# Kernel tuning notes

Hardware: AMD Instinct MI355X
Metric: run time of the kernel (lower is better)

The kernel has to match this reference:

```python
import jax, jax.numpy as jnp
import numpy as np


def _pairwise_iou(boxes):
    # boxes: [B, N, 4] in (x1, y1, x2, y2); returns IoU [B, N, N]
    area = (boxes[..., 2] - boxes[..., 0]) * (boxes[..., 3] - boxes[..., 1])  # [B, N]
    lt = jnp.maximum(boxes[:, :, None, :2], boxes[:, None, :, :2])  # [B, N, N, 2]
    rb = jnp.minimum(boxes[:, :, None, 2:], boxes[:, None, :, 2:])
    wh = jnp.clip(rb - lt, 0.0)
    inter = wh[..., 0] * wh[..., 1]  # [B, N, N]
    union = area[:, :, None] + area[:, None, :] - inter
    return inter / jnp.maximum(union, 1e-6)


def setup_inputs() -> dict:
    key = jax.random.key(0)
    kxy, kwh, ks = jax.random.split(key, 3)
    B, N, C = 4, 2048, 4
    xy = jax.random.uniform(kxy, (B, N, 2), dtype=jnp.float32) * 1000.0
    wh = jax.random.uniform(kwh, (B, N, 2), dtype=jnp.float32) * 100.0 + 1.0
    boxes = jnp.concatenate([xy, xy + wh], axis=-1)  # valid xyxy boxes
    scores = jax.random.uniform(ks, (B, C, N), dtype=jnp.float32)
    return {
        "boxes": boxes,
        "scores": scores,
        "iou_threshold": jnp.array([0.5], dtype=jnp.float32),
        "score_threshold": jnp.array([0.05], dtype=jnp.float32),
    }


def reference(boxes, scores, iou_threshold, score_threshold):
    # Greedy NMS-match (mmcv.ops.nms_match semantics), per batch and class.
    # Returns match: [B, C, N] int32 where match[b,c,n] is the index of the
    # group-leader (kept) box that box n belongs to, or -1 if unmatched
    # (i.e. score <= score_threshold).
    B, N, _ = boxes.shape
    C = scores.shape[1]
    thr = iou_threshold[0]
    sthr = score_threshold[0]

    iou = _pairwise_iou(boxes)  # [B, N, N] (shared across classes)
    order = jnp.argsort(-scores, axis=-1)  # [B, C, N], score-descending

    suppressed0 = scores <= sthr            # boxes below score threshold never match
    match0 = jnp.full((B, C, N), -1, jnp.int32)
    b_idx = jnp.arange(B)[:, None]          # [B, 1] for per-batch IoU row gather

    def step(carry, cand):
        # cand: [B, C] box index with next-highest score in each (batch, class)
        suppressed, match = carry           # [B, C, N] bool / int32
        cand_sup = jnp.take_along_axis(suppressed, cand[..., None], axis=-1)[..., 0]
        active = ~cand_sup                  # [B, C]: candidate not yet grouped
        cand_iou = iou[b_idx, cand]         # [B, C, N] IoU of candidate vs all boxes
        matched = active[..., None] & (~suppressed) & (cand_iou > thr)
        match = jnp.where(matched, cand[..., None].astype(jnp.int32), match)
        return (suppressed | matched, match), None

    xs = jnp.moveaxis(order, -1, 0)         # [N, B, C]: sequential greedy order
    (_, match), _ = jax.lax.scan(step, (suppressed0, match0), xs)
    return match
```

## Files before the change

### kernel.cpp

```cpp
#include <hip/hip_runtime.h>
#include <stdint.h>

#define N_   2048
#define NW   64
#define CLS  4
#define B_   4
#define ORD_STRIDE (N_ + 64)

__global__ __launch_bounds__(256) void build_mask(
    const float4* __restrict__ boxes, const float* __restrict__ thr_p,
    uint32_t* __restrict__ ov)
{
  __shared__ float4 sb[N_];
  const int b    = blockIdx.x >> 6;
  const int tile = blockIdx.x & 63;
  const float thr = thr_p[0];
  for (int i = threadIdx.x; i < N_; i += 256) sb[i] = boxes[b * N_ + i];
  __syncthreads();
  const int wv = threadIdx.x >> 6;
  const int ln = threadIdx.x & 63;
  const int r0 = tile * 32 + wv * 8;
  float4 bi[8]; float areai[8];
  #pragma unroll
  for (int rr = 0; rr < 8; ++rr) {
    bi[rr] = sb[r0 + rr];
    areai[rr] = (bi[rr].z - bi[rr].x) * (bi[rr].w - bi[rr].y);
  }
  uint32_t myw[8] = {0, 0, 0, 0, 0, 0, 0, 0};
  for (int g = 0; g < 32; ++g) {
    const float4 bj = sb[g * 64 + ln];
    const float areaj = (bj.z - bj.x) * (bj.w - bj.y);
    const bool sel = ((ln >> 1) == g);
    const bool hi  = (ln & 1);
    #pragma unroll
    for (int rr = 0; rr < 8; ++rr) {
      const float xx1 = fmaxf(bi[rr].x, bj.x);
      const float yy1 = fmaxf(bi[rr].y, bj.y);
      const float xx2 = fminf(bi[rr].z, bj.z);
      const float yy2 = fminf(bi[rr].w, bj.w);
      const float iw = fmaxf(xx2 - xx1, 0.0f);
      const float ih = fmaxf(yy2 - yy1, 0.0f);
      const float inter = iw * ih;
      const float uni = fmaxf(areai[rr] + areaj - inter, 1e-6f);
      const unsigned long long bal = __ballot(inter / uni > thr);
      const uint32_t w = hi ? (uint32_t)(bal >> 32) : (uint32_t)bal;
      if (sel) myw[rr] = w;
    }
  }
  #pragma unroll
  for (int rr = 0; rr < 8; ++rr)
    ov[((size_t)(b * N_ + r0 + rr)) * NW + ln] = myw[rr];
}

__global__ __launch_bounds__(256) void sort_init(
    const float* __restrict__ scores, const float* __restrict__ sthr_p,
    int* __restrict__ order, int* __restrict__ rk, uint32_t* __restrict__ sup0ws)
{
  __shared__ unsigned long long sp[N_];
  __shared__ uint32_t sup_l[NW];
  __shared__ int cnt_s;
  const int bc = blockIdx.x;
  const float sthr = sthr_p[0];
  const float* s = scores + (size_t)bc * N_;
  for (int i = threadIdx.x; i < N_; i += 256) {
    const float v = s[i];
    uint32_t u = __float_as_uint(v);
    u = (u >> 31) ? ~u : (u | 0x80000000u);
    sp[i] = ((unsigned long long)u << 32) | (uint32_t)(~(uint32_t)i);
    const unsigned long long bal = __ballot(v <= sthr);
    if ((threadIdx.x & 63) == 0) {
      sup_l[(i >> 5)]     = (uint32_t)bal;
      sup_l[(i >> 5) + 1] = (uint32_t)(bal >> 32);
    }
  }
  for (int size = 2; size <= N_; size <<= 1) {
    for (int stride = size >> 1; stride > 0; stride >>= 1) {
      __syncthreads();
      for (int t = threadIdx.x; t < N_ / 2; t += 256) {
        const int pos = 2 * t - (t & (stride - 1));
        const bool desc = ((t & (size >> 1)) == 0);
        const unsigned long long a = sp[pos], c = sp[pos + stride];
        if (desc != (a > c)) { sp[pos] = c; sp[pos + stride] = a; }
      }
    }
  }
  __syncthreads();
  if (threadIdx.x == 0) {
    int c2 = 0;
    for (int w = 0; w < NW; ++w) c2 += __popc(sup_l[w]);
    cnt_s = N_ - c2;
  }
  __syncthreads();
  const int cnt = cnt_s;
  const int last = (cnt > 0) ? (int)~(uint32_t)sp[cnt - 1] : 0;
  int* ord_o = order + (size_t)bc * ORD_STRIDE;
  int* rk_o  = rk    + (size_t)bc * N_;
  for (int i = threadIdx.x; i < N_; i += 256) {
    const int idx = (int)~(uint32_t)sp[i];
    ord_o[i] = (i < cnt || cnt == 0) ? idx : last;
    rk_o[idx] = i;
  }
  for (int i = N_ + threadIdx.x; i < ORD_STRIDE; i += 256) ord_o[i] = last;
  if (threadIdx.x < NW) sup0ws[bc * NW + threadIdx.x] = sup_l[threadIdx.x];
}


#define C_(r,b,s) \
  "v_and_b32 v36, v" #r ", v34\n\t"              \
  "v_lshlrev_b32 v38, 8, v" #s "\n\t"            \
  "v_cmp_ne_u32 s[46:47], 0, v36\n\t"            \
  "v_add_u32 v38, v38, v33\n\t"                  \
  "v_bfe_u32 v44, v" #s ", 5, 6\n\t"             \
  "s_and_b64 s[46:47], s[46:47], s[46:47]\n\t"   \
  "s_cselect_b32 s40, 0, -1\n\t"                 \
  "global_load_dword v" #r ", v38, %[B]\n\t"     \
  "v_and_b32 v37, s40, v" #b "\n\t"              \
  "v_or_b32 v34, v34, v37\n\t"                   \
  "v_cmp_eq_u32 s[48:49], v44, v32\n\t"          \
  "v_cndmask_b32 v37, 0, v45, s[48:49]\n\t"      \
  "v_lshlrev_b32 v" #b ", v" #s ", v37\n\t"

#define P_(r,b,s) \
  "v_lshlrev_b32 v38, 8, v" #s "\n\t"            \
  "v_add_u32 v38, v38, v33\n\t"                  \
  "global_load_dword v" #r ", v38, %[B]\n\t"     \
  "v_bfe_u32 v44, v" #s ", 5, 6\n\t"             \
  "v_cmp_eq_u32 s[48:49], v44, v32\n\t"          \
  "v_cndmask_b32 v37, 0, v45, s[48:49]\n\t"      \
  "v_lshlrev_b32 v" #b ", v" #s ", v37\n\t"

#define E_(r,b) \
  "v_and_b32 v36, v" #r ", v34\n\t"              \
  "v_cmp_ne_u32 s[46:47], 0, v36\n\t"            \
  "s_and_b64 s[46:47], s[46:47], s[46:47]\n\t"   \
  "s_cselect_b32 s40, 0, -1\n\t"                 \
  "v_and_b32 v37, s40, v" #b "\n\t"              \
  "v_or_b32 v34, v34, v37\n\t"

#define DSR0 \
  "ds_read_b128 v[144:147], v39\n\t"             \
  "ds_read_b128 v[148:151], v39 offset:16\n\t"   \
  "ds_read_b128 v[152:155], v39 offset:32\n\t"   \
  "ds_read_b128 v[156:159], v39 offset:48\n\t"   \
  "v_add_u32 v39, 64, v39\n\t"
#define DSR1 \
  "ds_read_b128 v[160:163], v39\n\t"             \
  "ds_read_b128 v[164:167], v39 offset:16\n\t"   \
  "ds_read_b128 v[168:171], v39 offset:32\n\t"   \
  "ds_read_b128 v[172:175], v39 offset:48\n\t"   \
  "v_add_u32 v39, 64, v39\n\t"
#define DSR2 \
  "ds_read_b128 v[176:179], v39\n\t"             \
  "ds_read_b128 v[180:183], v39 offset:16\n\t"   \
  "ds_read_b128 v[184:187], v39 offset:32\n\t"   \
  "ds_read_b128 v[188:191], v39 offset:48\n\t"   \
  "v_add_u32 v39, 64, v39\n\t"

#define CL_A \
  C_(96,48,144)  C_(97,49,145)  C_(98,50,146)  C_(99,51,147)  \
  C_(100,52,148) C_(101,53,149) C_(102,54,150) C_(103,55,151) \
  C_(104,56,152) C_(105,57,153) C_(106,58,154) C_(107,59,155) \
  C_(108,60,156) C_(109,61,157) C_(110,62,158) C_(111,63,159)
#define CL_B \
  C_(112,64,160) C_(113,65,161) C_(114,66,162) C_(115,67,163) \
  C_(116,68,164) C_(117,69,165) C_(118,70,166) C_(119,71,167) \
  C_(120,72,168) C_(121,73,169) C_(122,74,170) C_(123,75,171) \
  C_(124,76,172) C_(125,77,173) C_(126,78,174) C_(127,79,175)
#define CL_C \
  C_(128,80,176) C_(129,81,177) C_(130,82,178) C_(131,83,179) \
  C_(132,84,180) C_(133,85,181) C_(134,86,182) C_(135,87,183) \
  C_(136,88,184) C_(137,89,185) C_(138,90,186) C_(139,91,187) \
  C_(140,92,188) C_(141,93,189) C_(142,94,190) C_(143,95,191)

#define PL_A \
  P_(96,48,144)  P_(97,49,145)  P_(98,50,146)  P_(99,51,147)  \
  P_(100,52,148) P_(101,53,149) P_(102,54,150) P_(103,55,151) \
  P_(104,56,152) P_(105,57,153) P_(106,58,154) P_(107,59,155) \
  P_(108,60,156) P_(109,61,157) P_(110,62,158) P_(111,63,159)
#define PL_B \
  P_(112,64,160) P_(113,65,161) P_(114,66,162) P_(115,67,163) \
  P_(116,68,164) P_(117,69,165) P_(118,70,166) P_(119,71,167) \
  P_(120,72,168) P_(121,73,169) P_(122,74,170) P_(123,75,171) \
  P_(124,76,172) P_(125,77,173) P_(126,78,174) P_(127,79,175)
#define PL_C \
  P_(128,80,176) P_(129,81,177) P_(130,82,178) P_(131,83,179) \
  P_(132,84,180) P_(133,85,181) P_(134,86,182) P_(135,87,183) \
  P_(136,88,184) P_(137,89,185) P_(138,90,186) P_(139,91,187) \
  P_(140,92,188) P_(141,93,189) P_(142,94,190) P_(143,95,191)

#define EL_A \
  E_(96,48)  E_(97,49)  E_(98,50)  E_(99,51)  E_(100,52) E_(101,53) \
  E_(102,54) E_(103,55) E_(104,56) E_(105,57) E_(106,58) E_(107,59) \
  E_(108,60) E_(109,61) E_(110,62) E_(111,63)
#define EL_B \
  E_(112,64) E_(113,65) E_(114,66) E_(115,67) E_(116,68) E_(117,69) \
  E_(118,70) E_(119,71) E_(120,72) E_(121,73) E_(122,74) E_(123,75) \
  E_(124,76) E_(125,77) E_(126,78) E_(127,79)
#define EL_C \
  E_(128,80) E_(129,81) E_(130,82) E_(131,83) E_(132,84) E_(133,85) \
  E_(134,86) E_(135,87) E_(136,88) E_(137,89) E_(138,90) E_(139,91) \
  E_(140,92) E_(141,93) E_(142,94) E_(143,95)

#define PH_A "s_waitcnt vmcnt(32)\n\t" "s_waitcnt lgkmcnt(0)\n\t" DSR1 CL_A
#define PH_B "s_waitcnt vmcnt(32)\n\t" "s_waitcnt lgkmcnt(0)\n\t" DSR2 CL_B
#define PH_C "s_waitcnt vmcnt(32)\n\t" "s_waitcnt lgkmcnt(0)\n\t" DSR0 CL_C

__global__ __launch_bounds__(64, 1) void scan_lead(
    const int* __restrict__ order, const uint32_t* __restrict__ ov,
    uint32_t* __restrict__ leadws)
{
  __shared__ __align__(16) int sv[ORD_STRIDE];
  const int bc = blockIdx.x;
  const int b  = bc / CLS;
  const int l  = threadIdx.x;
  {
    const int4* src = (const int4*)(order + (size_t)bc * ORD_STRIDE);
    int4* dst = (int4*)sv;
    for (int i = l; i < ORD_STRIDE / 4; i += 64) dst[i] = src[i];
  }
  const int l4 = l << 2;
  const uint32_t cb = (uint32_t)(uintptr_t)(&sv[0]);
  const uint32_t* rowb = ov + (size_t)b * N_ * NW;
  uint32_t vlead;
  asm volatile(
    "s_waitcnt vmcnt(0) lgkmcnt(0)\n\t"
    "v_mov_b32 v32, %[LN]\n\t"
    "v_mov_b32 v33, %[L4]\n\t"
    "v_mov_b32 v34, 0\n\t"
    "v_mov_b32 v39, %[CB]\n\t"
    "v_mov_b32 v45, 1\n\t"
    DSR0 "s_waitcnt lgkmcnt(0)\n\t" PL_A
    DSR1 "s_waitcnt lgkmcnt(0)\n\t" PL_B
    DSR2 "s_waitcnt lgkmcnt(0)\n\t" PL_C
    DSR0
    "s_mov_b32 s41, 41\n\t"
    "LSCAN%=:\n\t"
    PH_A PH_B PH_C
    "s_sub_u32 s41, s41, 1\n\t"
    "s_cmp_lg_u32 s41, 0\n\t"
    "s_cbranch_scc1 LSCAN%=\n\t"
    PH_A PH_B
    "s_waitcnt vmcnt(32)\n\t" EL_C
    "s_waitcnt vmcnt(16)\n\t" EL_A
    "s_waitcnt vmcnt(0)\n\t"  EL_B
    "v_mov_b32 %[LD], v34\n\t"
    : [LD] "=v"(vlead)
    : [LN] "v"(l), [L4] "v"(l4), [CB] "v"(cb), [B] "s"(rowb)
    : "memory", "scc", "s40", "s41", "s46", "s47", "s48", "s49",
      "v32","v33","v34","v35","v36","v37","v38","v39","v44","v45",
      "v48","v49","v50","v51","v52","v53","v54","v55",
      "v56","v57","v58","v59","v60","v61","v62","v63","v64","v65","v66","v67",
      "v68","v69","v70","v71","v72","v73","v74","v75","v76","v77","v78","v79",
      "v80","v81","v82","v83","v84","v85","v86","v87","v88","v89","v90","v91",
      "v92","v93","v94","v95","v96","v97","v98","v99","v100","v101","v102","v103",
      "v104","v105","v106","v107","v108","v109","v110","v111","v112","v113","v114","v115",
      "v116","v117","v118","v119","v120","v121","v122","v123","v124","v125","v126","v127",
      "v128","v129","v130","v131","v132","v133","v134","v135","v136","v137","v138","v139",
      "v140","v141","v142","v143","v144","v145","v146","v147","v148","v149","v150","v151",
      "v152","v153","v154","v155","v156","v157","v158","v159","v160","v161","v162","v163",
      "v164","v165","v166","v167","v168","v169","v170","v171","v172","v173","v174","v175",
      "v176","v177","v178","v179","v180","v181","v182","v183","v184","v185","v186","v187",
      "v188","v189","v190","v191");
  leadws[bc * NW + l] = vlead;
}

__global__ __launch_bounds__(256) void extract_match(
    const uint32_t* __restrict__ ov, const int* __restrict__ rk,
    const uint32_t* __restrict__ sup0ws, const uint32_t* __restrict__ leadws,
    int* __restrict__ match)
{
  __shared__ __align__(16) int rk_s[N_];
  __shared__ uint32_t lead_s[NW];
  __shared__ uint32_t sup_s[NW];
  const int bc  = blockIdx.x >> 4;
  const int seg = blockIdx.x & 15;
  const int b   = bc / CLS;
  {
    const int4* src = (const int4*)(rk + (size_t)bc * N_);
    int4* dst = (int4*)rk_s;
    for (int i = threadIdx.x; i < N_ / 4; i += 256) dst[i] = src[i];
    if (threadIdx.x < NW) {
      lead_s[threadIdx.x] = leadws[bc * NW + threadIdx.x];
      sup_s[threadIdx.x]  = sup0ws[bc * NW + threadIdx.x];
    }
  }
  __syncthreads();
  const int wv = threadIdx.x >> 6;
  const int l  = threadIdx.x & 63;
  const uint32_t gl = lead_s[l];
  const uint32_t* Mb = ov + (size_t)b * N_ * NW;
  #pragma unroll 4
  for (int j = 0; j < 32; ++j) {
    const int n = seg * 128 + wv * 32 + j;
    uint32_t bits = Mb[(size_t)n * NW + l] & gl;
    int minp = 0x7FFFFFFF;
    while (bits) {
      const int k = __ffs(bits) - 1;
      bits &= bits - 1;
      const int jj = (l << 5) + k;
      const int pk = (rk_s[jj] << 11) | jj;
      minp = (pk < minp) ? pk : minp;
    }
    #pragma unroll
    for (int m = 32; m; m >>= 1) {
      const int o = __shfl_xor(minp, m);
      minp = (o < minp) ? o : minp;
    }
    const bool below = (sup_s[n >> 5] >> (n & 31)) & 1u;
    if (l == 0)
      match[(size_t)bc * N_ + n] =
          (below || minp == 0x7FFFFFFF) ? -1 : (minp & 2047);
  }
}

extern "C" void kernel_launch(void* const* d_in, const int* in_sizes, int n_in,
                              void* d_out, int out_size, void* d_ws, size_t ws_size,
                              hipStream_t stream)
{
  const float4* boxes  = (const float4*)d_in[0];
  const float*  scores = (const float*)d_in[1];
  const float*  iouthr = (const float*)d_in[2];
  const float*  scthr  = (const float*)d_in[3];
  int* match = (int*)d_out;

  char* ws = (char*)d_ws;
  uint32_t* ov    = (uint32_t*)ws;
  int*      order = (int*)(ws + (size_t)B_ * N_ * NW * 4);
  int*      rk    = (int*)((char*)order + (size_t)B_ * CLS * ORD_STRIDE * 4);
  uint32_t* sup0  = (uint32_t*)((char*)rk + (size_t)B_ * CLS * N_ * 4);
  uint32_t* leadw = (uint32_t*)((char*)sup0 + (size_t)B_ * CLS * NW * 4);

  build_mask   <<<dim3(256),      dim3(256), 0, stream>>>(boxes, iouthr, ov);
  sort_init    <<<dim3(B_ * CLS), dim3(256), 0, stream>>>(scores, scthr, order, rk, sup0);
  scan_lead    <<<dim3(B_ * CLS), dim3(64),  0, stream>>>(order, ov, leadw);
  extract_match<<<dim3(256),      dim3(256), 0, stream>>>(ov, rk, sup0, leadw, match);
}
```

Before: 196.0 us.

## Fuse sort, scan and match extraction into one kernel with leader-driven atomicMin scatter

Merges sort_init, scan_lead and extract_match into a single per-(batch,class) kernel that keeps order, rank and suppression data in shared memory, cutting two launches and the workspace round-trips. Match extraction now walks only the leader rows and scatters packed rank/index values into a shared array with atomicMin, instead of scanning every row against the leader mask. The inline scan also replaces the SALU select sequence with a vcc branch. In exchange, extraction runs on 16 blocks instead of 256, so it has much less parallelism, and shared-memory atomics may contend.

```diff
diff --git a/kernel.cpp b/kernel.cpp
--- a/kernel.cpp
+++ b/kernel.cpp
@@ -52,71 +52,18 @@
     ov[((size_t)(b * N_ + r0 + rr)) * NW + ln] = myw[rr];
 }
 
-__global__ __launch_bounds__(256) void sort_init(
-    const float* __restrict__ scores, const float* __restrict__ sthr_p,
-    int* __restrict__ order, int* __restrict__ rk, uint32_t* __restrict__ sup0ws)
-{
-  __shared__ unsigned long long sp[N_];
-  __shared__ uint32_t sup_l[NW];
-  __shared__ int cnt_s;
-  const int bc = blockIdx.x;
-  const float sthr = sthr_p[0];
-  const float* s = scores + (size_t)bc * N_;
-  for (int i = threadIdx.x; i < N_; i += 256) {
-    const float v = s[i];
-    uint32_t u = __float_as_uint(v);
-    u = (u >> 31) ? ~u : (u | 0x80000000u);
-    sp[i] = ((unsigned long long)u << 32) | (uint32_t)(~(uint32_t)i);
-    const unsigned long long bal = __ballot(v <= sthr);
-    if ((threadIdx.x & 63) == 0) {
-      sup_l[(i >> 5)]     = (uint32_t)bal;
-      sup_l[(i >> 5) + 1] = (uint32_t)(bal >> 32);
-    }
-  }
-  for (int size = 2; size <= N_; size <<= 1) {
-    for (int stride = size >> 1; stride > 0; stride >>= 1) {
-      __syncthreads();
-      for (int t = threadIdx.x; t < N_ / 2; t += 256) {
-        const int pos = 2 * t - (t & (stride - 1));
-        const bool desc = ((t & (size >> 1)) == 0);
-        const unsigned long long a = sp[pos], c = sp[pos + stride];
-        if (desc != (a > c)) { sp[pos] = c; sp[pos + stride] = a; }
-      }
-    }
-  }
-  __syncthreads();
-  if (threadIdx.x == 0) {
-    int c2 = 0;
-    for (int w = 0; w < NW; ++w) c2 += __popc(sup_l[w]);
-    cnt_s = N_ - c2;
-  }
-  __syncthreads();
-  const int cnt = cnt_s;
-  const int last = (cnt > 0) ? (int)~(uint32_t)sp[cnt - 1] : 0;
-  int* ord_o = order + (size_t)bc * ORD_STRIDE;
-  int* rk_o  = rk    + (size_t)bc * N_;
-  for (int i = threadIdx.x; i < N_; i += 256) {
-    const int idx = (int)~(uint32_t)sp[i];
-    ord_o[i] = (i < cnt || cnt == 0) ? idx : last;
-    rk_o[idx] = i;
-  }
-  for (int i = N_ + threadIdx.x; i < ORD_STRIDE; i += 256) ord_o[i] = last;
-  if (threadIdx.x < NW) sup0ws[bc * NW + threadIdx.x] = sup_l[threadIdx.x];
-}
-
 
 #define C_(r,b,s) \
   "v_and_b32 v36, v" #r ", v34\n\t"              \
   "v_lshlrev_b32 v38, 8, v" #s "\n\t"            \
-  "v_cmp_ne_u32 s[46:47], 0, v36\n\t"            \
+  "v_cmp_ne_u32 vcc, 0, v36\n\t"                 \
   "v_add_u32 v38, v38, v33\n\t"                  \
   "v_bfe_u32 v44, v" #s ", 5, 6\n\t"             \
-  "s_and_b64 s[46:47], s[46:47], s[46:47]\n\t"   \
-  "s_cselect_b32 s40, 0, -1\n\t"                 \
+  "v_cmp_eq_u32 s[48:49], v44, v32\n\t"          \
+  "s_cbranch_vccnz 1f\n\t"                       \
+  "v_or_b32 v34, v34, v" #b "\n\t"               \
+  "1:\n\t"                                       \
   "global_load_dword v" #r ", v38, %[B]\n\t"     \
-  "v_and_b32 v37, s40, v" #b "\n\t"              \
-  "v_or_b32 v34, v34, v37\n\t"                   \
-  "v_cmp_eq_u32 s[48:49], v44, v32\n\t"          \
   "v_cndmask_b32 v37, 0, v45, s[48:49]\n\t"      \
   "v_lshlrev_b32 v" #b ", v" #s ", v37\n\t"
 
@@ -131,11 +78,11 @@
 
 #define E_(r,b) \
   "v_and_b32 v36, v" #r ", v34\n\t"              \
-  "v_cmp_ne_u32 s[46:47], 0, v36\n\t"            \
-  "s_and_b64 s[46:47], s[46:47], s[46:47]\n\t"   \
-  "s_cselect_b32 s40, 0, -1\n\t"                 \
-  "v_and_b32 v37, s40, v" #b "\n\t"              \
-  "v_or_b32 v34, v34, v37\n\t"
+  "v_cmp_ne_u32 vcc, 0, v36\n\t"                 \
+  "s_nop 4\n\t"                                  \
+  "s_cbranch_vccnz 1f\n\t"                       \
+  "v_or_b32 v34, v34, v" #b "\n\t"               \
+  "1:\n\t"
 
 #define DSR0 \
   "ds_read_b128 v[144:147], v39\n\t"             \
@@ -205,111 +152,170 @@
 #define PH_B "s_waitcnt vmcnt(32)\n\t" "s_waitcnt lgkmcnt(0)\n\t" DSR2 CL_B
 #define PH_C "s_waitcnt vmcnt(32)\n\t" "s_waitcnt lgkmcnt(0)\n\t" DSR0 CL_C
 
-__global__ __launch_bounds__(64, 1) void scan_lead(
-    const int* __restrict__ order, const uint32_t* __restrict__ ov,
-    uint32_t* __restrict__ leadws)
+__global__ __launch_bounds__(256, 1) void nms_all(
+    const float* __restrict__ scores, const float* __restrict__ sthr_p,
+    const uint32_t* __restrict__ ov, int* __restrict__ match)
 {
+  __shared__ unsigned long long sp[N_];
   __shared__ __align__(16) int sv[ORD_STRIDE];
+  __shared__ __align__(16) int rk_s[N_];
+  __shared__ uint32_t sup_s[NW];
+  __shared__ uint32_t lead_s[NW];
+  __shared__ int cnt_s;
+  __shared__ int nl_s;
+
   const int bc = blockIdx.x;
   const int b  = bc / CLS;
-  const int l  = threadIdx.x;
-  {
-    const int4* src = (const int4*)(order + (size_t)bc * ORD_STRIDE);
-    int4* dst = (int4*)sv;
-    for (int i = l; i < ORD_STRIDE / 4; i += 64) dst[i] = src[i];
-  }
-  const int l4 = l << 2;
-  const uint32_t cb = (uint32_t)(uintptr_t)(&sv[0]);
+  const float sthr = sthr_p[0];
+  const float* s = scores + (size_t)bc * N_;
+
+  for (int i = threadIdx.x; i < N_; i += 256) {
+    const float v = s[i];
+    uint32_t u = __float_as_uint(v);
+    u = (u >> 31) ? ~u : (u | 0x80000000u);
+    sp[i] = ((unsigned long long)u << 32) | (uint32_t)(~(uint32_t)i);
+    const unsigned long long bal = __ballot(v <= sthr);
+    if ((threadIdx.x & 63) == 0) {
+      sup_s[(i >> 5)]     = (uint32_t)bal;
+      sup_s[(i >> 5) + 1] = (uint32_t)(bal >> 32);
+    }
+  }
+  for (int size = 2; size <= N_; size <<= 1) {
+    for (int stride = size >> 1; stride > 0; stride >>= 1) {
+      __syncthreads();
+      for (int t = threadIdx.x; t < N_ / 2; t += 256) {
+        const int pos = 2 * t - (t & (stride - 1));
+        const bool desc = ((t & (size >> 1)) == 0);
+        const unsigned long long a = sp[pos], c = sp[pos + stride];
+        if (desc != (a > c)) { sp[pos] = c; sp[pos + stride] = a; }
+      }
+    }
+  }
+  __syncthreads();
+  if (threadIdx.x == 0) {
+    int c2 = 0;
+    for (int w = 0; w < NW; ++w) c2 += __popc(sup_s[w]);
+    cnt_s = N_ - c2;
+    nl_s = 0;
+  }
+  __syncthreads();
+  const int cnt = cnt_s;
+  const int last = (cnt > 0) ? (int)~(uint32_t)sp[cnt - 1] : 0;
+  for (int i = threadIdx.x; i < N_; i += 256) {
+    const int idx = (int)~(uint32_t)sp[i];
+    sv[i] = (i < cnt || cnt == 0) ? idx : last;
+    rk_s[idx] = i;
+  }
+  for (int i = N_ + threadIdx.x; i < ORD_STRIDE; i += 256) sv[i] = last;
+  __syncthreads();
+
+  int* mm = (int*)sp;
   const uint32_t* rowb = ov + (size_t)b * N_ * NW;
-  uint32_t vlead;
-  asm volatile(
-    "s_waitcnt vmcnt(0) lgkmcnt(0)\n\t"
-    "v_mov_b32 v32, %[LN]\n\t"
-    "v_mov_b32 v33, %[L4]\n\t"
-    "v_mov_b32 v34, 0\n\t"
-    "v_mov_b32 v39, %[CB]\n\t"
-    "v_mov_b32 v45, 1\n\t"
-    DSR0 "s_waitcnt lgkmcnt(0)\n\t" PL_A
-    DSR1 "s_waitcnt lgkmcnt(0)\n\t" PL_B
-    DSR2 "s_waitcnt lgkmcnt(0)\n\t" PL_C
-    DSR0
-    "s_mov_b32 s41, 41\n\t"
-    "LSCAN%=:\n\t"
-    PH_A PH_B PH_C
-    "s_sub_u32 s41, s41, 1\n\t"
-    "s_cmp_lg_u32 s41, 0\n\t"
-    "s_cbranch_scc1 LSCAN%=\n\t"
-    PH_A PH_B
-    "s_waitcnt vmcnt(32)\n\t" EL_C
-    "s_waitcnt vmcnt(16)\n\t" EL_A
-    "s_waitcnt vmcnt(0)\n\t"  EL_B
-    "v_mov_b32 %[LD], v34\n\t"
-    : [LD] "=v"(vlead)
-    : [LN] "v"(l), [L4] "v"(l4), [CB] "v"(cb), [B] "s"(rowb)
-    : "memory", "scc", "s40", "s41", "s46", "s47", "s48", "s49",
-      "v32","v33","v34","v35","v36","v37","v38","v39","v44","v45",
-      "v48","v49","v50","v51","v52","v53","v54","v55",
-      "v56","v57","v58","v59","v60","v61","v62","v63","v64","v65","v66","v67",
-      "v68","v69","v70","v71","v72","v73","v74","v75","v76","v77","v78","v79",
-      "v80","v81","v82","v83","v84","v85","v86","v87","v88","v89","v90","v91",
-      "v92","v93","v94","v95","v96","v97","v98","v99","v100","v101","v102","v103",
-      "v104","v105","v106","v107","v108","v109","v110","v111","v112","v113","v114","v115",
-      "v116","v117","v118","v119","v120","v121","v122","v123","v124","v125","v126","v127",
-      "v128","v129","v130","v131","v132","v133","v134","v135","v136","v137","v138","v139",
-      "v140","v141","v142","v143","v144","v145","v146","v147","v148","v149","v150","v151",
-      "v152","v153","v154","v155","v156","v157","v158","v159","v160","v161","v162","v163",
-      "v164","v165","v166","v167","v168","v169","v170","v171","v172","v173","v174","v175",
-      "v176","v177","v178","v179","v180","v181","v182","v183","v184","v185","v186","v187",
-      "v188","v189","v190","v191");
-  leadws[bc * NW + l] = vlead;
-}
-
-__global__ __launch_bounds__(256) void extract_match(
-    const uint32_t* __restrict__ ov, const int* __restrict__ rk,
-    const uint32_t* __restrict__ sup0ws, const uint32_t* __restrict__ leadws,
-    int* __restrict__ match)
-{
-  __shared__ __align__(16) int rk_s[N_];
-  __shared__ uint32_t lead_s[NW];
-  __shared__ uint32_t sup_s[NW];
-  const int bc  = blockIdx.x >> 4;
-  const int seg = blockIdx.x & 15;
-  const int b   = bc / CLS;
-  {
-    const int4* src = (const int4*)(rk + (size_t)bc * N_);
-    int4* dst = (int4*)rk_s;
-    for (int i = threadIdx.x; i < N_ / 4; i += 256) dst[i] = src[i];
-    if (threadIdx.x < NW) {
-      lead_s[threadIdx.x] = leadws[bc * NW + threadIdx.x];
-      sup_s[threadIdx.x]  = sup0ws[bc * NW + threadIdx.x];
-    }
-  }
-  __syncthreads();
+  if (threadIdx.x < 64) {
+    const int l  = threadIdx.x;
+    const int l4 = l << 2;
+    const uint32_t cb = (uint32_t)(uintptr_t)(&sv[0]);
+    uint32_t vlead;
+    asm volatile(
+      "s_waitcnt vmcnt(0) lgkmcnt(0)\n\t"
+      "v_mov_b32 v32, %[LN]\n\t"
+      "v_mov_b32 v33, %[L4]\n\t"
+      "v_mov_b32 v34, 0\n\t"
+      "v_mov_b32 v39, %[CB]\n\t"
+      "v_mov_b32 v45, 1\n\t"
+      DSR0 "s_waitcnt lgkmcnt(0)\n\t" PL_A
+      DSR1 "s_waitcnt lgkmcnt(0)\n\t" PL_B
+      DSR2 "s_waitcnt lgkmcnt(0)\n\t" PL_C
+      DSR0
+      "s_mov_b32 s41, 41\n\t"
+      "LSCAN%=:\n\t"
+      PH_A PH_B PH_C
+      "s_sub_u32 s41, s41, 1\n\t"
+      "s_cmp_lg_u32 s41, 0\n\t"
+      "s_cbranch_scc1 LSCAN%=\n\t"
+      PH_A PH_B
+      "s_waitcnt vmcnt(32)\n\t" EL_C
+      "s_waitcnt vmcnt(16)\n\t" EL_A
+      "s_waitcnt vmcnt(0)\n\t"  EL_B
+      "v_mov_b32 %[LD], v34\n\t"
+      : [LD] "=v"(vlead)
+      : [LN] "v"(l), [L4] "v"(l4), [CB] "v"(cb), [B] "s"(rowb)
+      : "memory", "scc", "s40", "s41", "s46", "s47", "s48", "s49",
+        "v32","v33","v34","v35","v36","v37","v38","v39","v44","v45",
+        "v48","v49","v50","v51","v52","v53","v54","v55",
+        "v56","v57","v58","v59","v60","v61","v62","v63","v64","v65","v66","v67",
+        "v68","v69","v70","v71","v72","v73","v74","v75","v76","v77","v78","v79",
+        "v80","v81","v82","v83","v84","v85","v86","v87","v88","v89","v90","v91",
+        "v92","v93","v94","v95","v96","v97","v98","v99","v100","v101","v102","v103",
+        "v104","v105","v106","v107","v108","v109","v110","v111","v112","v113","v114","v115",
+        "v116","v117","v118","v119","v120","v121","v122","v123","v124","v125","v126","v127",
+        "v128","v129","v130","v131","v132","v133","v134","v135","v136","v137","v138","v139",
+        "v140","v141","v142","v143","v144","v145","v146","v147","v148","v149","v150","v151",
+        "v152","v153","v154","v155","v156","v157","v158","v159","v160","v161","v162","v163",
+        "v164","v165","v166","v167","v168","v169","v170","v171","v172","v173","v174","v175",
+        "v176","v177","v178","v179","v180","v181","v182","v183","v184","v185","v186","v187",
+        "v188","v189","v190","v191");
+    lead_s[l] = vlead;
+  } else {
+    for (int i = threadIdx.x - 64; i < N_; i += 192) mm[i] = 0x7FFFFFFF;
+  }
+  __syncthreads();
+
+  int* llist = sv;
+  for (int q = 0; q < 8; ++q) {
+    const int n = threadIdx.x * 8 + q;
+    if ((lead_s[n >> 5] >> (n & 31)) & 1u) {
+      const int p = atomicAdd(&nl_s, 1);
+      llist[p] = n;
+    }
+  }
+  __syncthreads();
+
+  const int L = nl_s;
   const int wv = threadIdx.x >> 6;
   const int l  = threadIdx.x & 63;
-  const uint32_t gl = lead_s[l];
-  const uint32_t* Mb = ov + (size_t)b * N_ * NW;
-  #pragma unroll 4
-  for (int j = 0; j < 32; ++j) {
-    const int n = seg * 128 + wv * 32 + j;
-    uint32_t bits = Mb[(size_t)n * NW + l] & gl;
-    int minp = 0x7FFFFFFF;
-    while (bits) {
-      const int k = __ffs(bits) - 1;
-      bits &= bits - 1;
-      const int jj = (l << 5) + k;
-      const int pk = (rk_s[jj] << 11) | jj;
-      minp = (pk < minp) ? pk : minp;
-    }
-    #pragma unroll
-    for (int m = 32; m; m >>= 1) {
-      const int o = __shfl_xor(minp, m);
-      minp = (o < minp) ? o : minp;
-    }
+  for (int i0 = wv; i0 < L; i0 += 16) {
+    const int i1 = i0 + 4, i2 = i0 + 8, i3 = i0 + 12;
+    const int la = llist[i0];
+    const int lb = (i1 < L) ? llist[i1] : la;
+    const int lc = (i2 < L) ? llist[i2] : la;
+    const int ld = (i3 < L) ? llist[i3] : la;
+    const uint32_t ra = rowb[(size_t)la * NW + l];
+    const uint32_t rb = (i1 < L) ? rowb[(size_t)lb * NW + l] : 0u;
+    const uint32_t rc = (i2 < L) ? rowb[(size_t)lc * NW + l] : 0u;
+    const uint32_t rd = (i3 < L) ? rowb[(size_t)ld * NW + l] : 0u;
+    {
+      const int pk = (rk_s[la] << 11) | la;
+      uint32_t bits = ra;
+      while (bits) { const int kk = __ffs(bits) - 1; bits &= bits - 1;
+        atomicMin(&mm[(l << 5) + kk], pk); }
+    }
+    {
+      const int pk = (rk_s[lb] << 11) | lb;
+      uint32_t bits = rb;
+      while (bits) { const int kk = __ffs(bits) - 1; bits &= bits - 1;
+        atomicMin(&mm[(l << 5) + kk], pk); }
+    }
+    {
+      const int pk = (rk_s[lc] << 11) | lc;
+      uint32_t bits = rc;
+      while (bits) { const int kk = __ffs(bits) - 1; bits &= bits - 1;
+        atomicMin(&mm[(l << 5) + kk], pk); }
+    }
+    {
+      const int pk = (rk_s[ld] << 11) | ld;
+      uint32_t bits = rd;
+      while (bits) { const int kk = __ffs(bits) - 1; bits &= bits - 1;
+        atomicMin(&mm[(l << 5) + kk], pk); }
+    }
+  }
+  __syncthreads();
+
+  for (int q = 0; q < 8; ++q) {
+    const int n = (q << 8) + threadIdx.x;
     const bool below = (sup_s[n >> 5] >> (n & 31)) & 1u;
-    if (l == 0)
-      match[(size_t)bc * N_ + n] =
-          (below || minp == 0x7FFFFFFF) ? -1 : (minp & 2047);
+    const int v = mm[n];
+    match[(size_t)bc * N_ + n] = (below || v == 0x7FFFFFFF) ? -1 : (v & 2047);
   }
 }
 
@@ -323,15 +329,8 @@
   const float*  scthr  = (const float*)d_in[3];
   int* match = (int*)d_out;
 
-  char* ws = (char*)d_ws;
-  uint32_t* ov    = (uint32_t*)ws;
-  int*      order = (int*)(ws + (size_t)B_ * N_ * NW * 4);
-  int*      rk    = (int*)((char*)order + (size_t)B_ * CLS * ORD_STRIDE * 4);
-  uint32_t* sup0  = (uint32_t*)((char*)rk + (size_t)B_ * CLS * N_ * 4);
-  uint32_t* leadw = (uint32_t*)((char*)sup0 + (size_t)B_ * CLS * NW * 4);
-
-  build_mask   <<<dim3(256),      dim3(256), 0, stream>>>(boxes, iouthr, ov);
-  sort_init    <<<dim3(B_ * CLS), dim3(256), 0, stream>>>(scores, scthr, order, rk, sup0);
-  scan_lead    <<<dim3(B_ * CLS), dim3(64),  0, stream>>>(order, ov, leadw);
-  extract_match<<<dim3(256),      dim3(256), 0, stream>>>(ov, rk, sup0, leadw, match);
+  uint32_t* ov = (uint32_t*)d_ws;
+
+  build_mask<<<dim3(256),      dim3(256), 0, stream>>>(boxes, iouthr, ov);
+  nms_all   <<<dim3(B_ * CLS), dim3(256), 0, stream>>>(scores, scthr, ov, match);
 }
```

Result: slower. 247.4 us (+26.2%).

## Merge mask build and sort kernels, and use branchy paired scan steps

Applied to the files above, without the earlier changes.

The IoU mask builder and the per-class bitonic sort now run in one 1024-thread launch, with different blocks taking each role. This removes a kernel boundary and lets the sort run alongside the mask work. Each sort thread now handles a single compare-exchange per stage. The scan loop's inline assembly processes candidates in pairs: it resolves the intra-pair dependency with a vector AND and replaces the scalar cselect masking with uniform vcc branches. This trades fewer instructions for branch overhead and manual s_nop hazard padding.

```diff
diff --git a/kernel.cpp b/kernel.cpp
--- a/kernel.cpp
+++ b/kernel.cpp
@@ -7,118 +7,147 @@
 #define B_   4
 #define ORD_STRIDE (N_ + 64)
 
-__global__ __launch_bounds__(256) void build_mask(
+__global__ __launch_bounds__(1024) void mask_or_sort(
     const float4* __restrict__ boxes, const float* __restrict__ thr_p,
-    uint32_t* __restrict__ ov)
+    const float* __restrict__ scores, const float* __restrict__ sthr_p,
+    uint32_t* __restrict__ ov, int* __restrict__ order,
+    int* __restrict__ rk, uint32_t* __restrict__ sup0ws)
 {
-  __shared__ float4 sb[N_];
-  const int b    = blockIdx.x >> 6;
-  const int tile = blockIdx.x & 63;
-  const float thr = thr_p[0];
-  for (int i = threadIdx.x; i < N_; i += 256) sb[i] = boxes[b * N_ + i];
-  __syncthreads();
-  const int wv = threadIdx.x >> 6;
-  const int ln = threadIdx.x & 63;
-  const int r0 = tile * 32 + wv * 8;
-  float4 bi[8]; float areai[8];
-  #pragma unroll
-  for (int rr = 0; rr < 8; ++rr) {
-    bi[rr] = sb[r0 + rr];
-    areai[rr] = (bi[rr].z - bi[rr].x) * (bi[rr].w - bi[rr].y);
-  }
-  uint32_t myw[8] = {0, 0, 0, 0, 0, 0, 0, 0};
-  for (int g = 0; g < 32; ++g) {
-    const float4 bj = sb[g * 64 + ln];
-    const float areaj = (bj.z - bj.x) * (bj.w - bj.y);
-    const bool sel = ((ln >> 1) == g);
-    const bool hi  = (ln & 1);
+  __shared__ __align__(16) unsigned char lds_raw[32768];
+  __shared__ uint32_t sup_l[NW];
+  __shared__ int cnt_s;
+
+  if (blockIdx.x < 64) {
+    float4* sb = (float4*)lds_raw;
+    const int b    = blockIdx.x >> 4;
+    const int tile = blockIdx.x & 15;
+    const float thr = thr_p[0];
+    for (int i = threadIdx.x; i < N_; i += 1024) sb[i] = boxes[b * N_ + i];
+    __syncthreads();
+    const int wv = threadIdx.x >> 6;
+    const int ln = threadIdx.x & 63;
+    const int r0 = tile * 128 + wv * 8;
+    float4 bi[8]; float areai[8];
     #pragma unroll
     for (int rr = 0; rr < 8; ++rr) {
-      const float xx1 = fmaxf(bi[rr].x, bj.x);
-      const float yy1 = fmaxf(bi[rr].y, bj.y);
-      const float xx2 = fminf(bi[rr].z, bj.z);
-      const float yy2 = fminf(bi[rr].w, bj.w);
-      const float iw = fmaxf(xx2 - xx1, 0.0f);
-      const float ih = fmaxf(yy2 - yy1, 0.0f);
-      const float inter = iw * ih;
-      const float uni = fmaxf(areai[rr] + areaj - inter, 1e-6f);
-      const unsigned long long bal = __ballot(inter / uni > thr);
-      const uint32_t w = hi ? (uint32_t)(bal >> 32) : (uint32_t)bal;
-      if (sel) myw[rr] = w;
-    }
-  }
-  #pragma unroll
-  for (int rr = 0; rr < 8; ++rr)
-    ov[((size_t)(b * N_ + r0 + rr)) * NW + ln] = myw[rr];
-}
-
-__global__ __launch_bounds__(256) void sort_init(
-    const float* __restrict__ scores, const float* __restrict__ sthr_p,
-    int* __restrict__ order, int* __restrict__ rk, uint32_t* __restrict__ sup0ws)
-{
-  __shared__ unsigned long long sp[N_];
-  __shared__ uint32_t sup_l[NW];
-  __shared__ int cnt_s;
-  const int bc = blockIdx.x;
-  const float sthr = sthr_p[0];
-  const float* s = scores + (size_t)bc * N_;
-  for (int i = threadIdx.x; i < N_; i += 256) {
-    const float v = s[i];
-    uint32_t u = __float_as_uint(v);
-    u = (u >> 31) ? ~u : (u | 0x80000000u);
-    sp[i] = ((unsigned long long)u << 32) | (uint32_t)(~(uint32_t)i);
-    const unsigned long long bal = __ballot(v <= sthr);
-    if ((threadIdx.x & 63) == 0) {
-      sup_l[(i >> 5)]     = (uint32_t)bal;
-      sup_l[(i >> 5) + 1] = (uint32_t)(bal >> 32);
-    }
-  }
-  for (int size = 2; size <= N_; size <<= 1) {
-    for (int stride = size >> 1; stride > 0; stride >>= 1) {
-      __syncthreads();
-      for (int t = threadIdx.x; t < N_ / 2; t += 256) {
+      bi[rr] = sb[r0 + rr];
+      areai[rr] = (bi[rr].z - bi[rr].x) * (bi[rr].w - bi[rr].y);
+    }
+    uint32_t myw[8] = {0, 0, 0, 0, 0, 0, 0, 0};
+    for (int g = 0; g < 32; ++g) {
+      const float4 bj = sb[g * 64 + ln];
+      const float areaj = (bj.z - bj.x) * (bj.w - bj.y);
+      const bool sel = ((ln >> 1) == g);
+      const bool hi  = (ln & 1);
+      #pragma unroll
+      for (int rr = 0; rr < 8; ++rr) {
+        const float xx1 = fmaxf(bi[rr].x, bj.x);
+        const float yy1 = fmaxf(bi[rr].y, bj.y);
+        const float xx2 = fminf(bi[rr].z, bj.z);
+        const float yy2 = fminf(bi[rr].w, bj.w);
+        const float iw = fmaxf(xx2 - xx1, 0.0f);
+        const float ih = fmaxf(yy2 - yy1, 0.0f);
+        const float inter = iw * ih;
+        const float uni = fmaxf(areai[rr] + areaj - inter, 1e-6f);
+        const unsigned long long bal = __ballot(inter / uni > thr);
+        const uint32_t w = hi ? (uint32_t)(bal >> 32) : (uint32_t)bal;
+        if (sel) myw[rr] = w;
+      }
+    }
+    #pragma unroll
+    for (int rr = 0; rr < 8; ++rr)
+      ov[((size_t)(b * N_ + r0 + rr)) * NW + ln] = myw[rr];
+  } else {
+    unsigned long long* sp = (unsigned long long*)lds_raw;
+    const int bc = blockIdx.x - 64;
+    const float sthr = sthr_p[0];
+    const float* s = scores + (size_t)bc * N_;
+    for (int i = threadIdx.x; i < N_; i += 1024) {
+      const float v = s[i];
+      uint32_t u = __float_as_uint(v);
+      u = (u >> 31) ? ~u : (u | 0x80000000u);
+      sp[i] = ((unsigned long long)u << 32) | (uint32_t)(~(uint32_t)i);
+      const unsigned long long bal = __ballot(v <= sthr);
+      if ((threadIdx.x & 63) == 0) {
+        sup_l[(i >> 5)]     = (uint32_t)bal;
+        sup_l[(i >> 5) + 1] = (uint32_t)(bal >> 32);
+      }
+    }
+    const int t = threadIdx.x;
+    for (int size = 2; size <= N_; size <<= 1) {
+      for (int stride = size >> 1; stride > 0; stride >>= 1) {
+        __syncthreads();
         const int pos = 2 * t - (t & (stride - 1));
         const bool desc = ((t & (size >> 1)) == 0);
         const unsigned long long a = sp[pos], c = sp[pos + stride];
         if (desc != (a > c)) { sp[pos] = c; sp[pos + stride] = a; }
       }
     }
+    __syncthreads();
+    if (threadIdx.x == 0) {
+      int c2 = 0;
+      for (int w = 0; w < NW; ++w) c2 += __popc(sup_l[w]);
+      cnt_s = N_ - c2;
+    }
+    __syncthreads();
+    const int cnt = cnt_s;
+    const int last = (cnt > 0) ? (int)~(uint32_t)sp[cnt - 1] : 0;
+    int* ord_o = order + (size_t)bc * ORD_STRIDE;
+    int* rk_o  = rk    + (size_t)bc * N_;
+    for (int i = threadIdx.x; i < N_; i += 1024) {
+      const int idx = (int)~(uint32_t)sp[i];
+      ord_o[i] = (i < cnt || cnt == 0) ? idx : last;
+      rk_o[idx] = i;
+    }
+    for (int i = N_ + threadIdx.x; i < ORD_STRIDE; i += 1024) ord_o[i] = last;
+    if (threadIdx.x < NW) sup0ws[bc * NW + threadIdx.x] = sup_l[threadIdx.x];
   }
-  __syncthreads();
-  if (threadIdx.x == 0) {
-    int c2 = 0;
-    for (int w = 0; w < NW; ++w) c2 += __popc(sup_l[w]);
-    cnt_s = N_ - c2;
-  }
-  __syncthreads();
-  const int cnt = cnt_s;
-  const int last = (cnt > 0) ? (int)~(uint32_t)sp[cnt - 1] : 0;
-  int* ord_o = order + (size_t)bc * ORD_STRIDE;
-  int* rk_o  = rk    + (size_t)bc * N_;
-  for (int i = threadIdx.x; i < N_; i += 256) {
-    const int idx = (int)~(uint32_t)sp[i];
-    ord_o[i] = (i < cnt || cnt == 0) ? idx : last;
-    rk_o[idx] = i;
-  }
-  for (int i = N_ + threadIdx.x; i < ORD_STRIDE; i += 256) ord_o[i] = last;
-  if (threadIdx.x < NW) sup0ws[bc * NW + threadIdx.x] = sup_l[threadIdx.x];
 }
 
 
-#define C_(r,b,s) \
-  "v_and_b32 v36, v" #r ", v34\n\t"              \
-  "v_lshlrev_b32 v38, 8, v" #s "\n\t"            \
-  "v_cmp_ne_u32 s[46:47], 0, v36\n\t"            \
+#define PAIR_(r1,b1,s1,r2,b2,s2) \
+  "v_and_b32 v36, v" #r1 ", v34\n\t"             \
+  "v_and_b32 v37, v" #r2 ", v34\n\t"             \
+  "v_and_b32 v35, v" #r2 ", v" #b1 "\n\t"        \
+  "v_cmp_ne_u32 vcc, 0, v36\n\t"                 \
+  "v_lshlrev_b32 v38, 8, v" #s1 "\n\t"           \
   "v_add_u32 v38, v38, v33\n\t"                  \
-  "v_bfe_u32 v44, v" #s ", 5, 6\n\t"             \
-  "s_and_b64 s[46:47], s[46:47], s[46:47]\n\t"   \
-  "s_cselect_b32 s40, 0, -1\n\t"                 \
-  "global_load_dword v" #r ", v38, %[B]\n\t"     \
-  "v_and_b32 v37, s40, v" #b "\n\t"              \
-  "v_or_b32 v34, v34, v37\n\t"                   \
+  "v_bfe_u32 v44, v" #s1 ", 5, 6\n\t"            \
+  "s_cbranch_vccnz 11f\n\t"                      \
+  "v_or_b32 v34, v34, v" #b1 "\n\t"              \
+  "v_or_b32 v37, v37, v35\n\t"                   \
+  "11:\n\t"                                      \
+  "global_load_dword v" #r1 ", v38, %[B]\n\t"    \
+  "v_cmp_ne_u32 vcc, 0, v37\n\t"                 \
   "v_cmp_eq_u32 s[48:49], v44, v32\n\t"          \
-  "v_cndmask_b32 v37, 0, v45, s[48:49]\n\t"      \
-  "v_lshlrev_b32 v" #b ", v" #s ", v37\n\t"
+  "v_lshlrev_b32 v38, 8, v" #s2 "\n\t"           \
+  "v_add_u32 v38, v38, v33\n\t"                  \
+  "v_cndmask_b32 v35, 0, v45, s[48:49]\n\t"      \
+  "s_cbranch_vccnz 12f\n\t"                      \
+  "v_or_b32 v34, v34, v" #b2 "\n\t"              \
+  "12:\n\t"                                      \
+  "global_load_dword v" #r2 ", v38, %[B]\n\t"    \
+  "v_lshlrev_b32 v" #b1 ", v" #s1 ", v35\n\t"    \
+  "v_bfe_u32 v44, v" #s2 ", 5, 6\n\t"            \
+  "v_cmp_eq_u32 s[48:49], v44, v32\n\t"          \
+  "v_cndmask_b32 v35, 0, v45, s[48:49]\n\t"      \
+  "v_lshlrev_b32 v" #b2 ", v" #s2 ", v35\n\t"
+
+#define EPAIR_(r1,b1,r2,b2) \
+  "v_and_b32 v36, v" #r1 ", v34\n\t"             \
+  "v_and_b32 v37, v" #r2 ", v34\n\t"             \
+  "v_and_b32 v35, v" #r2 ", v" #b1 "\n\t"        \
+  "v_cmp_ne_u32 vcc, 0, v36\n\t"                 \
+  "s_nop 4\n\t"                                  \
+  "s_cbranch_vccnz 13f\n\t"                      \
+  "v_or_b32 v34, v34, v" #b1 "\n\t"              \
+  "v_or_b32 v37, v37, v35\n\t"                   \
+  "13:\n\t"                                      \
+  "v_cmp_ne_u32 vcc, 0, v37\n\t"                 \
+  "s_nop 4\n\t"                                  \
+  "s_cbranch_vccnz 14f\n\t"                      \
+  "v_or_b32 v34, v34, v" #b2 "\n\t"              \
+  "14:\n\t"
 
 #define P_(r,b,s) \
   "v_lshlrev_b32 v38, 8, v" #s "\n\t"            \
@@ -128,14 +157,6 @@
   "v_cmp_eq_u32 s[48:49], v44, v32\n\t"          \
   "v_cndmask_b32 v37, 0, v45, s[48:49]\n\t"      \
   "v_lshlrev_b32 v" #b ", v" #s ", v37\n\t"
-
-#define E_(r,b) \
-  "v_and_b32 v36, v" #r ", v34\n\t"              \
-  "v_cmp_ne_u32 s[46:47], 0, v36\n\t"            \
-  "s_and_b64 s[46:47], s[46:47], s[46:47]\n\t"   \
-  "s_cselect_b32 s40, 0, -1\n\t"                 \
-  "v_and_b32 v37, s40, v" #b "\n\t"              \
-  "v_or_b32 v34, v34, v37\n\t"
 
 #define DSR0 \
   "ds_read_b128 v[144:147], v39\n\t"             \
@@ -156,22 +177,6 @@
   "ds_read_b128 v[188:191], v39 offset:48\n\t"   \
   "v_add_u32 v39, 64, v39\n\t"
 
-#define CL_A \
-  C_(96,48,144)  C_(97,49,145)  C_(98,50,146)  C_(99,51,147)  \
-  C_(100,52,148) C_(101,53,149) C_(102,54,150) C_(103,55,151) \
-  C_(104,56,152) C_(105,57,153) C_(106,58,154) C_(107,59,155) \
-  C_(108,60,156) C_(109,61,157) C_(110,62,158) C_(111,63,159)
-#define CL_B \
-  C_(112,64,160) C_(113,65,161) C_(114,66,162) C_(115,67,163) \
-  C_(116,68,164) C_(117,69,165) C_(118,70,166) C_(119,71,167) \
-  C_(120,72,168) C_(121,73,169) C_(122,74,170) C_(123,75,171) \
-  C_(124,76,172) C_(125,77,173) C_(126,78,174) C_(127,79,175)
-#define CL_C \
-  C_(128,80,176) C_(129,81,177) C_(130,82,178) C_(131,83,179) \
-  C_(132,84,180) C_(133,85,181) C_(134,86,182) C_(135,87,183) \
-  C_(136,88,184) C_(137,89,185) C_(138,90,186) C_(139,91,187) \
-  C_(140,92,188) C_(141,93,189) C_(142,94,190) C_(143,95,191)
-
 #define PL_A \
   P_(96,48,144)  P_(97,49,145)  P_(98,50,146)  P_(99,51,147)  \
   P_(100,52,148) P_(101,53,149) P_(102,54,150) P_(103,55,151) \
@@ -188,22 +193,36 @@
   P_(136,88,184) P_(137,89,185) P_(138,90,186) P_(139,91,187) \
   P_(140,92,188) P_(141,93,189) P_(142,94,190) P_(143,95,191)
 
+#define WAITS "s_waitcnt vmcnt(32)\n\t" "s_waitcnt lgkmcnt(0)\n\t"
+
+#define PH_A WAITS DSR1 \
+  PAIR_(96,48,144, 97,49,145)   PAIR_(98,50,146, 99,51,147)   \
+  PAIR_(100,52,148, 101,53,149) PAIR_(102,54,150, 103,55,151) \
+  PAIR_(104,56,152, 105,57,153) PAIR_(106,58,154, 107,59,155) \
+  PAIR_(108,60,156, 109,61,157) PAIR_(110,62,158, 111,63,159)
+#define PH_B WAITS DSR2 \
+  PAIR_(112,64,160, 113,65,161) PAIR_(114,66,162, 115,67,163) \
+  PAIR_(116,68,164, 117,69,165) PAIR_(118,70,166, 119,71,167) \
+  PAIR_(120,72,168, 121,73,169) PAIR_(122,74,170, 123,75,171) \
+  PAIR_(124,76,172, 125,77,173) PAIR_(126,78,174, 127,79,175)
+#define PH_C WAITS DSR0 \
+  PAIR_(128,80,176, 129,81,177) PAIR_(130,82,178, 131,83,179) \
+  PAIR_(132,84,180, 133,85,181) PAIR_(134,86,182, 135,87,183) \
+  PAIR_(136,88,184, 137,89,185) PAIR_(138,90,186, 139,91,187) \
+  PAIR_(140,92,188, 141,93,189) PAIR_(142,94,190, 143,95,191)
+
 #define EL_A \
-  E_(96,48)  E_(97,49)  E_(98,50)  E_(99,51)  E_(100,52) E_(101,53) \
-  E_(102,54) E_(103,55) E_(104,56) E_(105,57) E_(106,58) E_(107,59) \
-  E_(108,60) E_(109,61) E_(110,62) E_(111,63)
+  EPAIR_(96,48,97,49)   EPAIR_(98,50,99,51)   EPAIR_(100,52,101,53) \
+  EPAIR_(102,54,103,55) EPAIR_(104,56,105,57) EPAIR_(106,58,107,59) \
+  EPAIR_(108,60,109,61) EPAIR_(110,62,111,63)
 #define EL_B \
-  E_(112,64) E_(113,65) E_(114,66) E_(115,67) E_(116,68) E_(117,69) \
-  E_(118,70) E_(119,71) E_(120,72) E_(121,73) E_(122,74) E_(123,75) \
-  E_(124,76) E_(125,77) E_(126,78) E_(127,79)
+  EPAIR_(112,64,113,65) EPAIR_(114,66,115,67) EPAIR_(116,68,117,69) \
+  EPAIR_(118,70,119,71) EPAIR_(120,72,121,73) EPAIR_(122,74,123,75) \
+  EPAIR_(124,76,125,77) EPAIR_(126,78,127,79)
 #define EL_C \
-  E_(128,80) E_(129,81) E_(130,82) E_(131,83) E_(132,84) E_(133,85) \
-  E_(134,86) E_(135,87) E_(136,88) E_(137,89) E_(138,90) E_(139,91) \
-  E_(140,92) E_(141,93) E_(142,94) E_(143,95)
-
-#define PH_A "s_waitcnt vmcnt(32)\n\t" "s_waitcnt lgkmcnt(0)\n\t" DSR1 CL_A
-#define PH_B "s_waitcnt vmcnt(32)\n\t" "s_waitcnt lgkmcnt(0)\n\t" DSR2 CL_B
-#define PH_C "s_waitcnt vmcnt(32)\n\t" "s_waitcnt lgkmcnt(0)\n\t" DSR0 CL_C
+  EPAIR_(128,80,129,81) EPAIR_(130,82,131,83) EPAIR_(132,84,133,85) \
+  EPAIR_(134,86,135,87) EPAIR_(136,88,137,89) EPAIR_(138,90,139,91) \
+  EPAIR_(140,92,141,93) EPAIR_(142,94,143,95)
 
 __global__ __launch_bounds__(64, 1) void scan_lead(
     const int* __restrict__ order, const uint32_t* __restrict__ ov,
@@ -240,7 +259,7 @@
     "s_cmp_lg_u32 s41, 0\n\t"
     "s_cbranch_scc1 LSCAN%=\n\t"
     PH_A PH_B
-    "s_waitcnt vmcnt(32)\n\t" EL_C
+    "s_waitcnt vmcnt(32)\n\t" "s_waitcnt lgkmcnt(0)\n\t" EL_C
     "s_waitcnt vmcnt(16)\n\t" EL_A
     "s_waitcnt vmcnt(0)\n\t"  EL_B
     "v_mov_b32 %[LD], v34\n\t"
@@ -330,8 +349,8 @@
   uint32_t* sup0  = (uint32_t*)((char*)rk + (size_t)B_ * CLS * N_ * 4);
   uint32_t* leadw = (uint32_t*)((char*)sup0 + (size_t)B_ * CLS * NW * 4);
 
-  build_mask   <<<dim3(256),      dim3(256), 0, stream>>>(boxes, iouthr, ov);
-  sort_init    <<<dim3(B_ * CLS), dim3(256), 0, stream>>>(scores, scthr, order, rk, sup0);
+  mask_or_sort <<<dim3(64 + B_ * CLS), dim3(1024), 0, stream>>>(
+      boxes, iouthr, scores, scthr, ov, order, rk, sup0);
   scan_lead    <<<dim3(B_ * CLS), dim3(64),  0, stream>>>(order, ov, leadw);
   extract_match<<<dim3(256),      dim3(256), 0, stream>>>(ov, rk, sup0, leadw, match);
 }
```

After: 189.9 us. 1.03x faster.
